# Performance work log

Measured on AMD Instinct MI355X. Metric: run time of the kernel, lower is better.

The kernel has to match this reference:

```python
import jax, jax.numpy as jnp
import numpy as np

# V:N:M sparsity config (n=2 kept of m=8 per vector-block; mask pattern [1,0,1,0,0,0,0,0])
M_BLK = 8
KEEP_OFFSETS = np.array([0, 2], dtype=np.int32)  # positions kept in each m-block
B, S, D_IN, D_OUT = 2, 8192, 4096, 4096
K_KEPT = D_IN // M_BLK * len(KEEP_OFFSETS)  # 1024


def _keep_idx():
    # column indices of the surviving weight entries (same for every output row)
    blocks = np.arange(D_IN // M_BLK, dtype=np.int32)[:, None] * M_BLK  # [D_IN/M,1]
    return jnp.asarray((blocks + KEEP_OFFSETS[None, :]).reshape(-1))   # [K_KEPT]


def setup_inputs() -> dict:
    key = jax.random.key(0)
    k1, k2, k3 = jax.random.split(key, 3)
    x = jax.random.normal(k1, (B, S, D_IN), dtype=jnp.float32)
    values = jax.random.normal(k2, (D_OUT, K_KEPT), dtype=jnp.float32) * 0.02
    bias = jax.random.normal(k3, (D_OUT,), dtype=jnp.float32) * 0.02
    return {"x": x, "values": values, "bias": bias}


def reference(x, values, bias):
    # Sparse SpMM: gather kept input features, dense GEMM with compressed values.
    # Equivalent to x @ (masked dense W).T + bias, without materializing W.
    keep = _keep_idx()               # [K_KEPT] int32, constant metadata
    xg = x[..., keep]                # [B,S,K_KEPT]
    out = jnp.einsum('bsk,nk->bsn', xg, values) + bias  # [B,S,D_OUT]
    return out
```

## Files before the change

kernel.cpp:

```cpp
#include <hip/hip_runtime.h>
#include <hip/hip_bf16.h>


#define M_TOTAL 16384
#define DIN     4096
#define KDIM    1024
#define NDIM    4096

typedef unsigned short u16;
typedef unsigned int   u32;
typedef __bf16 bf16x8 __attribute__((ext_vector_type(8)));
typedef float  f32x4  __attribute__((ext_vector_type(4)));
typedef float  f32x16 __attribute__((ext_vector_type(16)));

typedef const void __attribute__((address_space(1)))* gp_t;
typedef void __attribute__((address_space(3)))*       lp_t;

__device__ __forceinline__ u16 f2bf(float f) {
    u32 u = __float_as_uint(f);
    u += 0x7FFFu + ((u >> 16) & 1u);
    return (u16)(u >> 16);
}
__device__ __forceinline__ u32 pack2(float a, float b) {
    return (u32)f2bf(a) | ((u32)f2bf(b) << 16);
}

__global__ void prep_kernel(const float* __restrict__ x, uint2* __restrict__ xg2,
                            const float* __restrict__ vals, uint4* __restrict__ vb4) {
    const int tid = threadIdx.x;
    if (blockIdx.x < 4096) {
        int i = blockIdx.x * 256 + tid;
        const int stride = 4096 * 256;
#pragma unroll
        for (int it = 0; it < 4; ++it, i += stride) {
            const f32x4* p = (const f32x4*)(x + (size_t)i * 16);
            f32x4 f0 = __builtin_nontemporal_load(p);
            f32x4 f1 = __builtin_nontemporal_load(p + 2);
            xg2[i] = make_uint2(pack2(f0.x, f0.z), pack2(f1.x, f1.z));
        }
    } else {
        const int i = (blockIdx.x - 4096) * 256 + tid;
        const f32x4* p = (const f32x4*)(vals + (size_t)i * 8);
        f32x4 a = __builtin_nontemporal_load(p);
        f32x4 b = __builtin_nontemporal_load(p + 1);
        vb4[i] = make_uint4(pack2(a.x, a.y), pack2(a.z, a.w),
                            pack2(b.x, b.y), pack2(b.z, b.w));
    }
}


#define LDSA(d, kh) (((d) * 2 + (kh)) * 16384)
#define LDSB(d, kh) (65536 + ((d) * 2 + (kh)) * 16384)

#define LOADA(d, kh, mh) { _Pragma("unroll") \
    for (int mm = 0; mm < 2; ++mm) { _Pragma("unroll") \
    for (int ks = 0; ks < 2; ++ks) \
        af[mm * 2 + ks] = *(const bf16x8*)(lds + LDSA(d, kh) \
            + (wr * 8 + ((mh) * 2 + mm) * 2) * 1024 + fl_base \
            + (((ks << 5) + acol) ^ aswz)); } }

#define LOADB(d, kh) { _Pragma("unroll") \
    for (int nn = 0; nn < 2; ++nn) { _Pragma("unroll") \
    for (int ks = 0; ks < 2; ++ks) \
        bfr[nn * 2 + ks] = *(const bf16x8*)(lds + LDSB(d, kh) \
            + (wc * 4 + nn * 2) * 1024 + fl_base \
            + (((ks << 5) + acol) ^ aswz)); } }

#define MFMA8(mh) { \
    __builtin_amdgcn_s_setprio(1); \
    _Pragma("unroll") for (int mm = 0; mm < 2; ++mm) \
    _Pragma("unroll") for (int nn = 0; nn < 2; ++nn) \
    _Pragma("unroll") for (int ks = 0; ks < 2; ++ks) \
        acc[(mh) * 2 + mm][nn] = __builtin_amdgcn_mfma_f32_32x32x16_bf16( \
            af[mm * 2 + ks], bfr[nn * 2 + ks], acc[(mh) * 2 + mm][nn], 0, 0, 0); \
    __builtin_amdgcn_s_setprio(0); }

#define BAR() __builtin_amdgcn_s_barrier()
#define VMCNT6() asm volatile("s_waitcnt vmcnt(6)" ::: "memory")

__global__ __launch_bounds__(512, 2) void gemm_kernel(
    const u16* __restrict__ A, const u16* __restrict__ Bv,
    const float* __restrict__ bias, float* __restrict__ C)
{
    __shared__ __align__(1024) char lds[131072];

    const int tid  = threadIdx.x;
    const int lane = tid & 63;
    const int wid  = tid >> 6;
    const int wr   = wid >> 2;
    const int wc   = wid & 3;

    const int bb   = blockIdx.x;
    const int btm0 = (bb & 7) * 8 + (bb >> 7);
    const int btn  = (bb >> 3) & 15;

    const int st_r0 = wid * 16 + (lane >> 2);
    const int st_ck = ((lane & 3) * 8) ^ ((tid & 32) >> 1) ^ ((tid & 64) >> 3);
    const u16* A0  = A  + (size_t)(btm0 * 256 + st_r0) * KDIM + st_ck;
    const u16* Bs0 = Bv + (size_t)(btn  * 256 + st_r0) * KDIM + st_ck;
    const int dst0 = tid * 16;

    const int fl_base = (lane & 15) * 64 + ((lane >> 4) & 1) * 1024;
    const int aswz    = (((lane >> 3) & 1) << 5) ^ (((lane >> 4) & 1) << 4);
    const int acol    = ((lane >> 5) & 1) * 16;

    auto STAGE = [&](const u16* as_, int s) {
        const int kt = s >> 2, j = s & 3;
        const int d = kt & 1, kh = (j >> 1) & 1;
        const int ko = kt * 64 + kh * 32;
        const u16* src = (j & 1) ? Bs0 : as_;
        const int base = ((j & 1) ? 65536 : 0) + (d * 2 + kh) * 16384;
        __builtin_amdgcn_global_load_lds((gp_t)(src + ko),
            (lp_t)(lds + base + dst0), 16, 0, 0);
        __builtin_amdgcn_global_load_lds((gp_t)(src + 128 * KDIM + ko),
            (lp_t)(lds + base + 8192 + dst0), 16, 0, 0);
    };

    const int c_colb = btn * 256 + wc * 64 + (lane & 31);
    float bvr[2];
#pragma unroll
    for (int n = 0; n < 2; ++n) bvr[n] = bias[c_colb + n * 32];

    f32x16 acc[4][2] = {};
    bf16x8 af[4], bfr[4];

    STAGE(A0, 0); STAGE(A0, 1); STAGE(A0, 2); STAGE(A0, 3);
    STAGE(A0, 4); STAGE(A0, 5); STAGE(A0, 6);
    VMCNT6();
    BAR();

#pragma unroll 1
    for (int r = 0; r < 4; ++r) {
        const u16* Ar = A0 + (size_t)r * 512 * KDIM;
        const u16* An = (r < 3) ? (Ar + 512 * KDIM) : Ar;

#pragma unroll 1
        for (int t = 0; t < 7; ++t) {
            const int s0 = 8 * t + 7;
            LOADB(0, 0); LOADA(0, 0, 0); STAGE(Ar, s0);     BAR(); MFMA8(0); BAR();
            LOADA(0, 0, 1);              STAGE(Ar, s0 + 1); BAR(); MFMA8(1); BAR();
            LOADB(0, 1); LOADA(0, 1, 0); STAGE(Ar, s0 + 2); BAR(); MFMA8(0); BAR();
            LOADA(0, 1, 1);              STAGE(Ar, s0 + 3); BAR(); MFMA8(1);
            VMCNT6(); BAR();
            LOADB(1, 0); LOADA(1, 0, 0); STAGE(Ar, s0 + 4); BAR(); MFMA8(0); BAR();
            LOADA(1, 0, 1);              STAGE(Ar, s0 + 5); BAR(); MFMA8(1); BAR();
            LOADB(1, 1); LOADA(1, 1, 0); STAGE(Ar, s0 + 6); BAR(); MFMA8(0); BAR();
            LOADA(1, 1, 1);              STAGE(Ar, s0 + 7); BAR(); MFMA8(1);
            VMCNT6(); BAR();
        }
        LOADB(0, 0); LOADA(0, 0, 0); STAGE(Ar, 63); BAR(); MFMA8(0); BAR();
        LOADA(0, 0, 1);              STAGE(An, 0);  BAR(); MFMA8(1); BAR();
        LOADB(0, 1); LOADA(0, 1, 0); STAGE(An, 1);  BAR(); MFMA8(0); BAR();
        LOADA(0, 1, 1);              STAGE(An, 2);  BAR(); MFMA8(1);
        VMCNT6(); BAR();
        LOADB(1, 0); LOADA(1, 0, 0); STAGE(An, 3);  BAR(); MFMA8(0); BAR();
        LOADA(1, 0, 1);              STAGE(An, 4);  BAR(); MFMA8(1); BAR();
        LOADB(1, 1); LOADA(1, 1, 0); STAGE(An, 5);  BAR(); MFMA8(0); BAR();
        LOADA(1, 1, 1);              STAGE(An, 6);  BAR(); MFMA8(1);
        VMCNT6(); BAR();

        const int c_row0 = (btm0 + 2 * r) * 256 + wr * 128 + ((lane >> 5) & 1) * 4;
#pragma unroll
        for (int mi = 0; mi < 4; ++mi) {
#pragma unroll
            for (int n = 0; n < 2; ++n) {
                f32x16 a = acc[mi][n];
#pragma unroll
                for (int q = 0; q < 4; ++q) {
#pragma unroll
                    for (int rr = 0; rr < 4; ++rr) {
                        const int row = c_row0 + mi * 32 + q * 8 + rr;
                        C[(size_t)row * NDIM + c_colb + n * 32] = a[q * 4 + rr] + bvr[n];
                    }
                }
#pragma unroll
                for (int z = 0; z < 16; ++z) acc[mi][n][z] = 0.f;
            }
        }
    }
}

extern "C" void kernel_launch(void* const* d_in, const int* in_sizes, int n_in,
                              void* d_out, int out_size, void* d_ws, size_t ws_size,
                              hipStream_t stream) {
    const float* x      = (const float*)d_in[0];
    const float* values = (const float*)d_in[1];
    const float* bias   = (const float*)d_in[2];
    float* out = (float*)d_out;

    u16* xg = (u16*)d_ws;
    u16* vb = (u16*)((char*)d_ws + ((size_t)32 << 20));

    prep_kernel<<<6144, 256, 0, stream>>>(x, (uint2*)xg, values, (uint4*)vb);
    gemm_kernel<<<256, 512, 0, stream>>>(xg, vb, bias, out);
}
```

Measured before the change: 207.4 us.

## Fuse gather/convert prep into persistent GEMM with flag-based overlap

Removes the separate prep kernel and does the bf16 gather/convert of x and values inside the GEMM kernel. Only the first two row-sets of x plus all of values are converted up front, followed by a grid-wide atomic barrier. The remaining x conversion is interleaved into the GEMM main loop, with per-round global flags that order producers and consumers. This aims to hide the memory-bound conversion behind MFMA work, but it relies on all 256 blocks being co-resident and adds spin-waits, fences, extra register pressure and a memset launch.

```diff
diff --git a/kernel.cpp b/kernel.cpp
--- a/kernel.cpp
+++ b/kernel.cpp
@@ -2,8 +2,6 @@
 #include <hip/hip_bf16.h>
 
 
-#define M_TOTAL 16384
-#define DIN     4096
 #define KDIM    1024
 #define NDIM    4096
 
@@ -24,30 +22,7 @@
 __device__ __forceinline__ u32 pack2(float a, float b) {
     return (u32)f2bf(a) | ((u32)f2bf(b) << 16);
 }
-
-__global__ void prep_kernel(const float* __restrict__ x, uint2* __restrict__ xg2,
-                            const float* __restrict__ vals, uint4* __restrict__ vb4) {
-    const int tid = threadIdx.x;
-    if (blockIdx.x < 4096) {
-        int i = blockIdx.x * 256 + tid;
-        const int stride = 4096 * 256;
-#pragma unroll
-        for (int it = 0; it < 4; ++it, i += stride) {
-            const f32x4* p = (const f32x4*)(x + (size_t)i * 16);
-            f32x4 f0 = __builtin_nontemporal_load(p);
-            f32x4 f1 = __builtin_nontemporal_load(p + 2);
-            xg2[i] = make_uint2(pack2(f0.x, f0.z), pack2(f1.x, f1.z));
-        }
-    } else {
-        const int i = (blockIdx.x - 4096) * 256 + tid;
-        const f32x4* p = (const f32x4*)(vals + (size_t)i * 8);
-        f32x4 a = __builtin_nontemporal_load(p);
-        f32x4 b = __builtin_nontemporal_load(p + 1);
-        vb4[i] = make_uint4(pack2(a.x, a.y), pack2(a.z, a.w),
-                            pack2(b.x, b.y), pack2(b.z, b.w));
-    }
-}
-
+#define NT(p) __builtin_nontemporal_load(p)
 
 #define LDSA(d, kh) (((d) * 2 + (kh)) * 16384)
 #define LDSB(d, kh) (65536 + ((d) * 2 + (kh)) * 16384)
@@ -77,10 +52,26 @@
 
 #define BAR() __builtin_amdgcn_s_barrier()
 #define VMCNT6() asm volatile("s_waitcnt vmcnt(6)" ::: "memory")
-
-__global__ __launch_bounds__(512, 2) void gemm_kernel(
-    const u16* __restrict__ A, const u16* __restrict__ Bv,
-    const float* __restrict__ bias, float* __restrict__ C)
+#define VMCNT0() asm volatile("s_waitcnt vmcnt(0)" ::: "memory")
+
+#define CLUMP_L(o) { \
+    const int p_ = 8 * (jc >> 9) + ((jc >> 8) & 1) + 2 * (r + 2); \
+    const float* xb_ = x + (size_t)(256 * p_ + (jc & 255)) * 4096 + (li0 + (o)) * 16; \
+    _Pragma("unroll") for (int jj = 0; jj < 4; ++jj) { \
+        pld[2 * jj]     = NT((const f32x4*)(xb_ + jj * 16)); \
+        pld[2 * jj + 1] = NT((const f32x4*)(xb_ + jj * 16 + 8)); } }
+
+#define CLUMP_S(o) { \
+    const int p_ = 8 * (jc >> 9) + ((jc >> 8) & 1) + 2 * (r + 2); \
+    const size_t gr_ = (size_t)(256 * p_ + (jc & 255)) * 256 + li0 + (o); \
+    _Pragma("unroll") for (int jj = 0; jj < 4; ++jj) \
+        xg2[gr_ + jj] = make_uint2(pack2(pld[2 * jj].x, pld[2 * jj].z), \
+                                   pack2(pld[2 * jj + 1].x, pld[2 * jj + 1].z)); }
+
+__global__ __launch_bounds__(512, 2) void fused_kernel(
+    const float* __restrict__ x, const float* __restrict__ vals,
+    const float* __restrict__ bias, u16* __restrict__ xg,
+    u16* __restrict__ vb, u32* __restrict__ flags, float* __restrict__ C)
 {
     __shared__ __align__(1024) char lds[131072];
 
@@ -89,15 +80,49 @@
     const int wid  = tid >> 6;
     const int wr   = wid >> 2;
     const int wc   = wid & 3;
-
     const int bb   = blockIdx.x;
+
+    uint2* xg2 = (uint2*)xg;
+    uint4* vb4 = (uint4*)vb;
+    const int g = bb * 512 + tid;
+
+#pragma unroll
+    for (int it = 0; it < 4; ++it) {
+        const int i = g + it * 131072;
+        const f32x4* p = (const f32x4*)(vals + (size_t)i * 8);
+        f32x4 a = NT(p), b = NT(p + 1);
+        vb4[i] = make_uint4(pack2(a.x, a.y), pack2(a.z, a.w),
+                            pack2(b.x, b.y), pack2(b.z, b.w));
+    }
+#pragma unroll 1
+    for (int it = 0; it < 16; ++it) {
+        const int u = g + it * 131072;
+        const int set = u >> 20, us = u & 1048575;
+        const int j_ = us >> 8, li = us & 255;
+        const int p_ = 8 * (j_ >> 9) + ((j_ >> 8) & 1) + 2 * set;
+        const size_t xrow = (size_t)(256 * p_ + (j_ & 255));
+        const float* q = x + xrow * 4096 + li * 16;
+        f32x4 a = NT((const f32x4*)q), b = NT((const f32x4*)(q + 8));
+        xg2[xrow * 256 + li] = make_uint2(pack2(a.x, a.z), pack2(b.x, b.z));
+    }
+    VMCNT0();
+    __threadfence();
+    __syncthreads();
+    if (tid == 0) {
+        __hip_atomic_fetch_add(&flags[0], 1u, __ATOMIC_RELEASE, __HIP_MEMORY_SCOPE_AGENT);
+        while (__hip_atomic_load(&flags[0], __ATOMIC_ACQUIRE, __HIP_MEMORY_SCOPE_AGENT) < 256u)
+            __builtin_amdgcn_s_sleep(8);
+    }
+    __syncthreads();
+    __threadfence();
+
     const int btm0 = (bb & 7) * 8 + (bb >> 7);
     const int btn  = (bb >> 3) & 15;
 
     const int st_r0 = wid * 16 + (lane >> 2);
     const int st_ck = ((lane & 3) * 8) ^ ((tid & 32) >> 1) ^ ((tid & 64) >> 3);
-    const u16* A0  = A  + (size_t)(btm0 * 256 + st_r0) * KDIM + st_ck;
-    const u16* Bs0 = Bv + (size_t)(btn  * 256 + st_r0) * KDIM + st_ck;
+    const u16* A0  = xg + (size_t)(btm0 * 256 + st_r0) * KDIM + st_ck;
+    const u16* Bs0 = vb + (size_t)(btn  * 256 + st_r0) * KDIM + st_ck;
     const int dst0 = tid * 16;
 
     const int fl_base = (lane & 15) * 64 + ((lane >> 4) & 1) * 1024;
@@ -121,8 +146,13 @@
 #pragma unroll
     for (int n = 0; n < 2; ++n) bvr[n] = bias[c_colb + n * 32];
 
+    const size_t ubase = (size_t)g * 8;
+    const int jc  = (int)(ubase >> 8);
+    const int li0 = (int)(ubase & 255);
+
     f32x16 acc[4][2] = {};
     bf16x8 af[4], bfr[4];
+    f32x4 pld[8];
 
     STAGE(A0, 0); STAGE(A0, 1); STAGE(A0, 2); STAGE(A0, 3);
     STAGE(A0, 4); STAGE(A0, 5); STAGE(A0, 6);
@@ -136,6 +166,25 @@
 
 #pragma unroll 1
         for (int t = 0; t < 7; ++t) {
+            if (t == 2 && r < 2) { CLUMP_L(0) }
+            if (t == 3 && r < 2) { CLUMP_S(0) CLUMP_L(4) }
+            if (t == 4 && r < 2) { CLUMP_S(4) }
+            if (t == 5 && r < 3) {
+                VMCNT0();
+                __threadfence();
+                BAR();
+                if (tid == 0) {
+                    if (r < 2)
+                        __hip_atomic_fetch_add(&flags[2 + r], 1u, __ATOMIC_RELEASE,
+                                               __HIP_MEMORY_SCOPE_AGENT);
+                    if (r >= 1)
+                        while (__hip_atomic_load(&flags[1 + r], __ATOMIC_ACQUIRE,
+                                                 __HIP_MEMORY_SCOPE_AGENT) < 256u)
+                            __builtin_amdgcn_s_sleep(8);
+                }
+                BAR();
+                __threadfence();
+            }
             const int s0 = 8 * t + 7;
             LOADB(0, 0); LOADA(0, 0, 0); STAGE(Ar, s0);     BAR(); MFMA8(0); BAR();
             LOADA(0, 0, 1);              STAGE(Ar, s0 + 1); BAR(); MFMA8(1); BAR();
@@ -188,9 +237,10 @@
     const float* bias   = (const float*)d_in[2];
     float* out = (float*)d_out;
 
-    u16* xg = (u16*)d_ws;
-    u16* vb = (u16*)((char*)d_ws + ((size_t)32 << 20));
-
-    prep_kernel<<<6144, 256, 0, stream>>>(x, (uint2*)xg, values, (uint4*)vb);
-    gemm_kernel<<<256, 512, 0, stream>>>(xg, vb, bias, out);
-}
+    u16* xg    = (u16*)d_ws;
+    u16* vb    = (u16*)((char*)d_ws + ((size_t)32 << 20));
+    u32* flags = (u32*)((char*)d_ws + ((size_t)40 << 20));
+
+    hipMemsetAsync(flags, 0, 64, stream);
+    fused_kernel<<<256, 512, 0, stream>>>(x, values, bias, xg, vb, flags, out);
+}
```

After: 623.0 us. 3x slower.
